# Kernel optimization log

Measured on AMD Instinct MI355X. Metric: run time of the kernel, lower is better.

## Reference

```python
import jax, jax.numpy as jnp
import numpy as np

N, E, IN_FEATS, D, H, DIST_DIM, NBOUND = 10000, 160000, 128, 64, 4, 32, 31

def setup_inputs() -> dict:
    key = jax.random.key(0)
    ks = jax.random.split(key, 16)
    gain = 5.0 / 3.0  # tanh gain
    def xavier(k, shape):
        # xavier_normal over the last two dims (fan_in, fan_out) as torch does per-slice
        fan_in, fan_out = shape[-2], shape[-1]
        std = gain * np.sqrt(2.0 / (fan_in + fan_out))
        return jax.random.normal(k, shape, dtype=jnp.float32) * std
    inp = {
        'feat': jax.random.normal(ks[0], (N, IN_FEATS), dtype=jnp.float32),
        'locations': jax.random.normal(ks[1], (N, 3), dtype=jnp.float32),
        'src': jax.random.randint(ks[2], (E,), 0, N),
        'dst': jax.random.randint(ks[3], (E,), 0, N),
        'inter_ids': jax.random.randint(ks[4], (E, H), 0, N),
        'W_fc': xavier(ks[5], (IN_FEATS, H * D)),
        'embed_table': jax.random.normal(ks[6], (NBOUND + 1, DIST_DIM), dtype=jnp.float32),
        'G': xavier(ks[7], (H, DIST_DIM, D)),
        'attn_fc1': xavier(ks[8], (H, 2 * D, D)),
        'attn_fc2': xavier(ks[9], (H, 2 * D, D)),
        'attn_fc3': xavier(ks[10], (H, 2 * D, D)),
        'attn_fc': xavier(ks[11], (H, 3 * D, D)),
        'attn_out': xavier(ks[12], (H, D, 1)),
        'boundaries': jnp.linspace(0.1, 3.1, NBOUND).astype(jnp.float32),
    }
    return inp


def reference(feat, locations, W_fc, embed_table, G, attn_fc1, attn_fc2, attn_fc3,
              attn_fc, attn_out, boundaries, src, dst, inter_ids):
    n = feat.shape[0]
    h = (feat @ W_fc).reshape(n, H, D)                      # [N,H,D]
    pos = locations                                          # [N,3]
    src_pos = pos[src]                                       # [E,3]
    dst_pos = pos[dst]                                       # [E,3]
    inter_pos = pos[inter_ids]                               # [E,H,3]
    h_src = h[src]                                           # [E,H,D]
    h_dst = h[dst]                                           # [E,H,D]
    head_idx = jnp.arange(H)[None, :]
    inter_h = h[inter_ids, head_idx, :]                      # [E,H,D] per-head gather

    e_count = src.shape[0]
    dist1 = jnp.broadcast_to(jnp.linalg.norm(dst_pos - src_pos, axis=-1)[:, None], (e_count, H))
    dist2 = jnp.linalg.norm(dst_pos[:, None, :] - inter_pos, axis=-1)   # [E,H]
    dist_ = jnp.linalg.norm(src_pos[:, None, :] - inter_pos, axis=-1)   # [E,H]

    def dist_embed(dist):
        idx = jnp.searchsorted(boundaries, dist, side='left')  # torch.bucketize(right=False)
        e = embed_table[idx]                                   # [E,H,DIST_DIM]
        return jnp.einsum('ehk,hkd->ehd', e, G)                # [E,H,D]

    de1 = dist_embed(dist1)
    de2 = dist_embed(dist2)
    de_ = dist_embed(dist_)

    d1 = jnp.einsum('ehk,hkd->ehd', jnp.concatenate([h_src, de1], axis=-1), attn_fc1)
    d2 = jnp.einsum('ehk,hkd->ehd', jnp.concatenate([inter_h, de2], axis=-1), attn_fc2)
    d3 = jnp.einsum('ehk,hkd->ehd', jnp.concatenate([h_dst, de_], axis=-1), attn_fc3)

    h_c = jnp.tanh(jnp.einsum('ehk,hkd->ehd', jnp.concatenate([d1, d2, d3], axis=-1), attn_fc))
    e_score = jnp.einsum('ehd,hdo->eho', h_c, attn_out)[..., 0]        # [E,H]

    # edge softmax grouped by destination node
    m = jax.ops.segment_max(e_score, dst, num_segments=n)              # [N,H]
    ex = jnp.exp(e_score - m[dst])
    den = jax.ops.segment_sum(ex, dst, num_segments=n)                 # [N,H]
    a = ex / den[dst]                                                  # [E,H]

    ft = jax.ops.segment_sum(a[:, :, None] * h_src, dst, num_segments=n)  # [N,H,D]
    rst = jnp.mean(ft, axis=1)                                          # merge='mean' -> [N,D]
    return rst
```

## Files before the change

kernel.cpp:

```cpp
#include <hip/hip_runtime.h>
#include <hip/hip_fp16.h>
#include <math.h>

#define N_NODES 10000
#define E_EDGES 160000
#define DMODEL 64
#define H 4
#define NBOUND 31
#define SLOTS 64
#define QREC 1024

typedef _Float16 half8 __attribute__((ext_vector_type(8)));
typedef float floatx4 __attribute__((ext_vector_type(4)));

__device__ __forceinline__ void mm4(const float* __restrict__ S, int aoff,
                                    int astride, int boff, int i0, int j,
                                    int Kdim, float o[4]) {
  float a0 = 0.f, a1 = 0.f, a2 = 0.f, a3 = 0.f;
  for (int t4 = 0; t4 < (Kdim >> 2); ++t4) {
    float4 f0 = *(const float4*)&S[aoff + (i0 + 0) * astride + t4 * 4];
    float4 f1 = *(const float4*)&S[aoff + (i0 + 1) * astride + t4 * 4];
    float4 f2 = *(const float4*)&S[aoff + (i0 + 2) * astride + t4 * 4];
    float4 f3 = *(const float4*)&S[aoff + (i0 + 3) * astride + t4 * 4];
    float b0 = S[boff + (t4 * 4 + 0) * 64 + j];
    float b1 = S[boff + (t4 * 4 + 1) * 64 + j];
    float b2 = S[boff + (t4 * 4 + 2) * 64 + j];
    float b3 = S[boff + (t4 * 4 + 3) * 64 + j];
    a0 += f0.x * b0 + f0.y * b1 + f0.z * b2 + f0.w * b3;
    a1 += f1.x * b0 + f1.y * b1 + f1.z * b2 + f1.w * b3;
    a2 += f2.x * b0 + f2.y * b1 + f2.z * b2 + f2.w * b3;
    a3 += f3.x * b0 + f3.y * b1 + f3.z * b2 + f3.w * b3;
  }
  o[0] = a0; o[1] = a1; o[2] = a2; o[3] = a3;
}

__device__ __forceinline__ int didx(const float* __restrict__ bnd2, float d) {
  int g = (int)(d * 10.0f);
  g = (g < 0) ? 0 : ((g > 31) ? 31 : g);
  g += (bnd2[g + 1] < d) ? 1 : 0;
  g -= (bnd2[g] >= d) ? 1 : 0;
  return g;
}

__global__ __launch_bounds__(512) void prep_kernel(
    const float* __restrict__ fc1, const float* __restrict__ fc2,
    const float* __restrict__ fc3, const float* __restrict__ fcc,
    const float* __restrict__ Wfc, const float* __restrict__ G,
    const float* __restrict__ emb, __half* __restrict__ bigWT,
    __half* __restrict__ U16, int* __restrict__ cnt) {
  __shared__ __align__(16) float S[12288];
  int bi = blockIdx.x;
  int tid = threadIdx.x;
  if (bi >= 24) {
    int n = (bi - 24) * 512 + tid;
    if (n < N_NODES) cnt[n] = 0;
    return;
  }
  int chain = (bi >= 12);
  int kh = chain ? (bi - 12) : bi;
  int k = kh >> 2, h = kh & 3;
  const float* fck = (k == 0) ? fc1 : (k == 1) ? fc2 : fc3;
  fck += h * 128 * 64;
  const float* F = fcc + h * 192 * 64 + k * 64 * 64;
  int j = tid & 63, ig = tid >> 6;
  float o[4];
  if (!chain) {
    #pragma unroll
    for (int u = 0; u < 2; ++u) {
      ((float4*)S)[u * 512 + tid] = ((const float4*)F)[u * 512 + tid];
      ((float4*)(S + 4096))[u * 512 + tid] = ((const float4*)fck)[u * 512 + tid];
    }
    __syncthreads();
    #pragma unroll
    for (int rg = 0; rg < 2; ++rg) {
      int i0 = ig * 8 + rg * 4;
      mm4(S, 4096, 64, 0, i0, j, 64, o);
      S[8192 + (i0 + 0) * 64 + j] = o[0];
      S[8192 + (i0 + 1) * 64 + j] = o[1];
      S[8192 + (i0 + 2) * 64 + j] = o[2];
      S[8192 + (i0 + 3) * 64 + j] = o[3];
    }
    __syncthreads();
    #pragma unroll
    for (int u = 0; u < 2; ++u) {
      int fi = u * 512 + tid;
      int i = fi >> 4, c4 = fi & 15;
      ((float4*)(S + 4096))[fi] = ((const float4*)(Wfc + i * 256 + h * 64))[c4];
    }
    __syncthreads();
    if (k == 0) {
      #pragma unroll
      for (int u = 0; u < 8; ++u) {
        int idx = u * 512 + tid;
        int i = idx >> 6, jj = idx & 63;
        bigWT[(h * 64 + jj) * 128 + i] = __float2half(S[4096 + idx]);
      }
    }
    #pragma unroll
    for (int rg = 0; rg < 2; ++rg) {
      int i0 = ig * 8 + rg * 4;
      mm4(S, 4096, 64, 8192, i0, j, 64, o);
      int rb = ((k + 1) * 256 + h * 64 + j) * 128;
      bigWT[rb + i0 + 0] = __float2half(o[0]);
      bigWT[rb + i0 + 1] = __float2half(o[1]);
      bigWT[rb + i0 + 2] = __float2half(o[2]);
      bigWT[rb + i0 + 3] = __float2half(o[3]);
    }
    __syncthreads();
    #pragma unroll
    for (int u = 0; u < 2; ++u) {
      int fi = u * 512 + tid;
      int i = fi >> 4, c4 = fi & 15;
      ((float4*)(S + 4096))[fi] =
          ((const float4*)(Wfc + (64 + i) * 256 + h * 64))[c4];
    }
    __syncthreads();
    if (k == 0) {
      #pragma unroll
      for (int u = 0; u < 8; ++u) {
        int idx = u * 512 + tid;
        int i = idx >> 6, jj = idx & 63;
        bigWT[(h * 64 + jj) * 128 + 64 + i] = __float2half(S[4096 + idx]);
      }
    }
    #pragma unroll
    for (int rg = 0; rg < 2; ++rg) {
      int i0 = ig * 8 + rg * 4;
      mm4(S, 4096, 64, 8192, i0, j, 64, o);
      int rb = ((k + 1) * 256 + h * 64 + j) * 128;
      bigWT[rb + 64 + i0 + 0] = __float2half(o[0]);
      bigWT[rb + 64 + i0 + 1] = __float2half(o[1]);
      bigWT[rb + 64 + i0 + 2] = __float2half(o[2]);
      bigWT[rb + 64 + i0 + 3] = __float2half(o[3]);
    }
    return;
  }
  #pragma unroll
  for (int u = 0; u < 2; ++u) {
    ((float4*)S)[u * 512 + tid] = ((const float4*)F)[u * 512 + tid];
    ((float4*)(S + 4096))[u * 512 + tid] =
        ((const float4*)(fck + 4096))[u * 512 + tid];
  }
  __syncthreads();
  #pragma unroll
  for (int rg = 0; rg < 2; ++rg) {
    int i0 = ig * 8 + rg * 4;
    mm4(S, 4096, 64, 0, i0, j, 64, o);
    S[8192 + (i0 + 0) * 64 + j] = o[0];
    S[8192 + (i0 + 1) * 64 + j] = o[1];
    S[8192 + (i0 + 2) * 64 + j] = o[2];
    S[8192 + (i0 + 3) * 64 + j] = o[3];
  }
  __syncthreads();
  ((float4*)S)[tid] = ((const float4*)(G + h * 2048))[tid];
  if (tid < 256) ((float4*)(S + 2048))[tid] = ((const float4*)emb)[tid];
  __syncthreads();
  {
    int i0 = ig * 4;
    mm4(S, 0, 64, 8192, i0, j, 64, o);
    S[3072 + (i0 + 0) * 64 + j] = o[0];
    S[3072 + (i0 + 1) * 64 + j] = o[1];
    S[3072 + (i0 + 2) * 64 + j] = o[2];
    S[3072 + (i0 + 3) * 64 + j] = o[3];
  }
  __syncthreads();
  {
    int i0 = ig * 4;
    mm4(S, 2048, 32, 3072, i0, j, 32, o);
    int base = k * 8192 + h * 2048;
    U16[base + (i0 + 0) * 64 + j] = __float2half(o[0]);
    U16[base + (i0 + 1) * 64 + j] = __float2half(o[1]);
    U16[base + (i0 + 2) * 64 + j] = __float2half(o[2]);
    U16[base + (i0 + 3) * 64 + j] = __float2half(o[3]);
  }
}

#define EROW 264

__global__ __launch_bounds__(256) void gemm_edge_kernel(
    const float* __restrict__ feat, const __half* __restrict__ bigWT,
    __half* __restrict__ qall, const float* __restrict__ pos,
    const int* __restrict__ src, const int* __restrict__ dst,
    const int* __restrict__ inter, const float* __restrict__ boundaries,
    int* __restrict__ cnt, uint4* __restrict__ ebuf) {
  __shared__ __align__(16) __half Esm[4][16][EROW];
  __shared__ float Sb[48];
  int bi = blockIdx.x;
  int tid = threadIdx.x;
  if (bi >= 628) {
    if (tid < NBOUND) Sb[tid + 1] = boundaries[tid];
    if (tid == NBOUND) { Sb[0] = -INFINITY; Sb[32] = INFINITY; }
    __syncthreads();
    int e = (bi - 628) * 256 + tid;
    int s = src[e], t = dst[e];
    int4 iv = *(const int4*)&inter[e * 4];
    int itarr[4] = {iv.x, iv.y, iv.z, iv.w};
    float sx = pos[s * 3], sy = pos[s * 3 + 1], sz = pos[s * 3 + 2];
    float tx = pos[t * 3], ty = pos[t * 3 + 1], tz = pos[t * 3 + 2];
    float dx = tx - sx, dy = ty - sy, dz = tz - sz;
    float dist1 = sqrtf(dx * dx + dy * dy + dz * dz);
    unsigned i1 = (unsigned)didx(Sb, dist1);
    unsigned w3 = 0, q20 = 0, q_0 = 0;
    #pragma unroll
    for (int hh = 0; hh < 4; ++hh) {
      int it = itarr[hh];
      float ix = pos[it * 3], iy = pos[it * 3 + 1], iz = pos[it * 3 + 2];
      float ax = tx - ix, ay = ty - iy, az = tz - iz;
      float dist2 = sqrtf(ax * ax + ay * ay + az * az);
      float bx = sx - ix, by = sy - iy, bz = sz - iz;
      float dist_ = sqrtf(bx * bx + by * by + bz * bz);
      unsigned idx2 = (unsigned)didx(Sb, dist2);
      unsigned idx_ = (unsigned)didx(Sb, dist_);
      if (hh == 0) { q20 = idx2; q_0 = idx_; }
      else w3 |= (idx2 | (idx_ << 5)) << ((hh - 1) * 10);
    }
    uint4 rec;
    rec.x = (unsigned)s | ((unsigned)itarr[0] << 16);
    rec.y = (unsigned)itarr[1] | ((unsigned)itarr[2] << 16);
    rec.z = (unsigned)itarr[3] | (i1 << 16) | (q20 << 21) | (q_0 << 26);
    rec.w = w3;
    int p = atomicAdd(&cnt[t], 1);
    if (p < SLOTS) ebuf[t * SLOTS + p] = rec;
    return;
  }
  int bx = bi % 157, by = bi / 157;
  int wv = tid >> 6, l = tid & 63;
  int m0 = bx * 64 + wv * 16;
  int n0 = by * 256;
  int lm = l & 15, lk = (l >> 4) * 8;
  int arow = m0 + lm;
  if (arow >= N_NODES) arow = N_NODES - 1;
  const float* fp = feat + arow * 128 + lk;
  const _Float16* bp = (const _Float16*)bigWT + lk;
  half8 a[4];
  #pragma unroll
  for (int kt = 0; kt < 4; ++kt) {
    float4 u0 = *(const float4*)(fp + kt * 32);
    float4 u1 = *(const float4*)(fp + kt * 32 + 4);
    half8 t;
    t[0] = (_Float16)u0.x; t[1] = (_Float16)u0.y;
    t[2] = (_Float16)u0.z; t[3] = (_Float16)u0.w;
    t[4] = (_Float16)u1.x; t[5] = (_Float16)u1.y;
    t[6] = (_Float16)u1.z; t[7] = (_Float16)u1.w;
    a[kt] = t;
  }
  #pragma unroll
  for (int nt = 0; nt < 16; ++nt) {
    floatx4 acc = (floatx4){0.f, 0.f, 0.f, 0.f};
    #pragma unroll
    for (int kt = 0; kt < 4; ++kt) {
      half8 b = *(const half8*)(bp + (n0 + nt * 16 + lm) * 128 + kt * 32);
      acc = __builtin_amdgcn_mfma_f32_16x16x32_f16(a[kt], b, acc, 0, 0, 0);
    }
    int dd = nt * 16 + lm;
    int o = (by == 0) ? ((dd & 63) * 4 + (dd >> 6)) : dd;
    #pragma unroll
    for (int r4 = 0; r4 < 4; ++r4)
      Esm[wv][(l >> 4) * 4 + r4][o] = __float2half(acc[r4]);
  }
  __syncthreads();
  int row = l >> 2;
  int j0 = (l & 3) * 64;
  int m = m0 + row;
  if (m < N_NODES) {
    #pragma unroll
    for (int u = 0; u < 8; ++u) {
      uint4 v = *(const uint4*)&Esm[wv][row][j0 + u * 8];
      *(uint4*)&qall[m * QREC + by * 256 + j0 + u * 8] = v;
    }
  }
}

__device__ __forceinline__ float dpp_row_sum16(float v) {
  int x;
  x = __builtin_amdgcn_update_dpp(0, __float_as_int(v), 0x128, 0xf, 0xf, true);
  v += __int_as_float(x);
  x = __builtin_amdgcn_update_dpp(0, __float_as_int(v), 0x124, 0xf, 0xf, true);
  v += __int_as_float(x);
  x = __builtin_amdgcn_update_dpp(0, __float_as_int(v), 0x122, 0xf, 0xf, true);
  v += __int_as_float(x);
  x = __builtin_amdgcn_update_dpp(0, __float_as_int(v), 0x121, 0xf, 0xf, true);
  v += __int_as_float(x);
  return v;
}

union H4u { uint2 u; __half2 h[2]; };

__device__ __forceinline__ float tanh_dot(H4u A, H4u B, H4u C, H4u X, H4u Y,
                                          H4u Z, float4 a4) {
  __half2 z0 = __hadd2(__hadd2(A.h[0], B.h[0]), __hadd2(C.h[0], X.h[0]));
  z0 = __hadd2(z0, __hadd2(Y.h[0], Z.h[0]));
  __half2 z1 = __hadd2(__hadd2(A.h[1], B.h[1]), __hadd2(C.h[1], X.h[1]));
  z1 = __hadd2(z1, __hadd2(Y.h[1], Z.h[1]));
  float2 f0 = __half22float2(z0);
  float2 f1 = __half22float2(z1);
  const float K = 2.885390082f;
  float p0 = __builtin_amdgcn_exp2f(f0.x * K);
  float p1 = __builtin_amdgcn_exp2f(f0.y * K);
  float p2 = __builtin_amdgcn_exp2f(f1.x * K);
  float p3 = __builtin_amdgcn_exp2f(f1.y * K);
  float r0 = __builtin_amdgcn_rcpf(p0 + 1.0f);
  float r1 = __builtin_amdgcn_rcpf(p1 + 1.0f);
  float r2 = __builtin_amdgcn_rcpf(p2 + 1.0f);
  float r3 = __builtin_amdgcn_rcpf(p3 + 1.0f);
  float dot = a4.x * r0;
  dot = fmaf(a4.y, r1, dot);
  dot = fmaf(a4.z, r2, dot);
  dot = fmaf(a4.w, r3, dot);
  float asum = (a4.x + a4.y) + (a4.z + a4.w);
  return fmaf(-2.0f, dot, asum);
}

__device__ __forceinline__ float4 h4_to_f4(uint2 u) {
  union { uint2 ui; __half2 h[2]; } cc;
  cc.ui = u;
  float2 a = __half22float2(cc.h[0]);
  float2 b = __half22float2(cc.h[1]);
  return make_float4(a.x, a.y, b.x, b.y);
}

__device__ __forceinline__ void dec_rec(uint4 r, int h, int* s, int* it,
                                        unsigned* i1, unsigned* q2,
                                        unsigned* q_) {
  *s = (int)(r.x & 0xffff);
  *it = (h == 0) ? (int)(r.x >> 16)
      : (h == 1) ? (int)(r.y & 0xffff)
      : (h == 2) ? (int)(r.y >> 16) : (int)(r.z & 0xffff);
  *i1 = (r.z >> 16) & 31;
  if (h == 0) {
    *q2 = (r.z >> 21) & 31;
    *q_ = (r.z >> 26) & 31;
  } else {
    unsigned f = r.w >> ((h - 1) * 10);
    *q2 = f & 31;
    *q_ = (f >> 5) & 31;
  }
}

__device__ __forceinline__ void gather_edge(
    const __half* __restrict__ qall, const __half* __restrict__ U16, int h,
    int c, int lane, int s, int it, unsigned i1, unsigned q2, unsigned q_,
    H4u* A, H4u* B, H4u* X, H4u* Y, H4u* Z, uint2* hr) {
  A->u = *(const uint2*)(qall + s * QREC + 256 + h * 64 + c * 4);
  B->u = *(const uint2*)(qall + it * QREC + 512 + h * 64 + c * 4);
  X->u = *(const uint2*)(U16 + (h * 32 + (int)i1) * 64 + c * 4);
  Y->u = *(const uint2*)(U16 + 8192 + (h * 32 + (int)q2) * 64 + c * 4);
  Z->u = *(const uint2*)(U16 + 16384 + (h * 32 + (int)q_) * 64 + c * 4);
  *hr = *(const uint2*)(qall + s * QREC + lane * 4);
}

__global__ __launch_bounds__(256) void score_agg_kernel(
    const int* __restrict__ cnt, const uint4* __restrict__ ebuf,
    const __half* __restrict__ qall, const __half* __restrict__ U16,
    const float* __restrict__ aout, float* __restrict__ out) {
  __shared__ uint4 recs[SLOTS];
  __shared__ float4 sm_num[4][64];
  __shared__ float4 sm_den[4];
  int tid = threadIdx.x;
  int w = tid >> 6, lane = tid & 63;
  int h = lane >> 4, c = lane & 15;
  int n = blockIdx.x;
  int deg = cnt[n];
  if (deg > SLOTS) deg = SLOTS;
  if (tid < deg) recs[tid] = ebuf[n * SLOTS + tid];
  H4u C;
  C.u = *(const uint2*)(qall + n * QREC + 768 + h * 64 + c * 4);
  const float4 a4 = *((const float4*)(aout + h * 64) + c);
  __syncthreads();
  float4 num = make_float4(0.f, 0.f, 0.f, 0.f);
  float4 den = make_float4(0.f, 0.f, 0.f, 0.f);
  for (int i = w; i < deg; i += 8) {
    int iB = i + 4;
    int vB = (iB < deg);
    uint4 rA = recs[i];
    uint4 rB = recs[vB ? iB : i];
    int sA, itA, sB, itB;
    unsigned i1A, q2A, q_A, i1B, q2B, q_B;
    dec_rec(rA, h, &sA, &itA, &i1A, &q2A, &q_A);
    dec_rec(rB, h, &sB, &itB, &i1B, &q2B, &q_B);
    H4u A0, B0, X0, Y0, Z0, A1, B1, X1, Y1, Z1;
    uint2 hr0, hr1;
    gather_edge(qall, U16, h, c, lane, sA, itA, i1A, q2A, q_A, &A0, &B0, &X0,
                &Y0, &Z0, &hr0);
    gather_edge(qall, U16, h, c, lane, sB, itB, i1B, q2B, q_B, &A1, &B1, &X1,
                &Y1, &Z1, &hr1);
    float v0 = tanh_dot(A0, B0, C, X0, Y0, Z0, a4);
    float v1 = tanh_dot(A1, B1, C, X1, Y1, Z1, a4);
    v0 = dpp_row_sum16(v0);
    v1 = dpp_row_sum16(v1);
    float ex0 = __expf(v0);
    float ex1 = vB ? __expf(v1) : 0.f;
    float4 hv0 = h4_to_f4(hr0);
    float4 hv1 = h4_to_f4(hr1);
    float e00 = __shfl(ex0, 0), e01 = __shfl(ex0, 16);
    float e02 = __shfl(ex0, 32), e03 = __shfl(ex0, 48);
    float e10 = __shfl(ex1, 0), e11 = __shfl(ex1, 16);
    float e12 = __shfl(ex1, 32), e13 = __shfl(ex1, 48);
    num.x += e00 * hv0.x + e10 * hv1.x;
    num.y += e01 * hv0.y + e11 * hv1.y;
    num.z += e02 * hv0.z + e12 * hv1.z;
    num.w += e03 * hv0.w + e13 * hv1.w;
    den.x += e00 + e10;
    den.y += e01 + e11;
    den.z += e02 + e12;
    den.w += e03 + e13;
  }
  sm_num[w][lane] = num;
  if (lane == 0) sm_den[w] = den;
  __syncthreads();
  if (tid < 64) {
    float4 n0 = sm_num[0][tid], n1 = sm_num[1][tid];
    float4 n2 = sm_num[2][tid], n3 = sm_num[3][tid];
    float4 d0 = sm_den[0], d1 = sm_den[1], d2 = sm_den[2], d3 = sm_den[3];
    float4 ns = make_float4(n0.x + n1.x + n2.x + n3.x, n0.y + n1.y + n2.y + n3.y,
                            n0.z + n1.z + n2.z + n3.z, n0.w + n1.w + n2.w + n3.w);
    float4 ds = make_float4(d0.x + d1.x + d2.x + d3.x, d0.y + d1.y + d2.y + d3.y,
                            d0.z + d1.z + d2.z + d3.z, d0.w + d1.w + d2.w + d3.w);
    float r = 0.f;
    if (deg > 0)
      r = 0.25f * (ns.x / ds.x + ns.y / ds.y + ns.z / ds.z + ns.w / ds.w);
    out[n * 64 + tid] = r;
  }
}

extern "C" void kernel_launch(void* const* d_in, const int* in_sizes, int n_in,
                              void* d_out, int out_size, void* d_ws,
                              size_t ws_size, hipStream_t stream) {
  const float* feat = (const float*)d_in[0];
  const float* loc = (const float*)d_in[1];
  const int* src = (const int*)d_in[2];
  const int* dst = (const int*)d_in[3];
  const int* inter = (const int*)d_in[4];
  const float* Wfc = (const float*)d_in[5];
  const float* emb = (const float*)d_in[6];
  const float* G = (const float*)d_in[7];
  const float* fc1 = (const float*)d_in[8];
  const float* fc2 = (const float*)d_in[9];
  const float* fc3 = (const float*)d_in[10];
  const float* fcc = (const float*)d_in[11];
  const float* aout = (const float*)d_in[12];
  const float* bnd = (const float*)d_in[13];
  float* out = (float*)d_out;

  __half* qall = (__half*)d_ws;
  __half* bigWT = qall + N_NODES * QREC;
  __half* U16 = bigWT + 1024 * 128;
  uint4* ebuf = (uint4*)(U16 + 3 * H * 2048);
  int* cnt = (int*)(ebuf + N_NODES * SLOTS);

  prep_kernel<<<44, 512, 0, stream>>>(fc1, fc2, fc3, fcc, Wfc, G, emb, bigWT,
                                      U16, cnt);
  gemm_edge_kernel<<<1253, 256, 0, stream>>>(feat, bigWT, qall, loc, src, dst,
                                             inter, bnd, cnt, ebuf);
  score_agg_kernel<<<N_NODES, 256, 0, stream>>>(cnt, ebuf, qall, U16, aout,
                                                out);
}
```

Measured before the change: 174.4 us.

## Interleave source features with projections, pad positions, per-lane head aggregation

```diff
diff --git a/kernel.cpp b/kernel.cpp
--- a/kernel.cpp
+++ b/kernel.cpp
@@ -46,14 +46,18 @@
     const float* __restrict__ fc1, const float* __restrict__ fc2,
     const float* __restrict__ fc3, const float* __restrict__ fcc,
     const float* __restrict__ Wfc, const float* __restrict__ G,
-    const float* __restrict__ emb, __half* __restrict__ bigWT,
-    __half* __restrict__ U16, int* __restrict__ cnt) {
+    const float* __restrict__ emb, const float* __restrict__ pos,
+    __half* __restrict__ bigWT, __half* __restrict__ U16,
+    int* __restrict__ cnt, float4* __restrict__ pos4) {
   __shared__ __align__(16) float S[12288];
   int bi = blockIdx.x;
   int tid = threadIdx.x;
   if (bi >= 24) {
     int n = (bi - 24) * 512 + tid;
-    if (n < N_NODES) cnt[n] = 0;
+    if (n < N_NODES) {
+      cnt[n] = 0;
+      pos4[n] = make_float4(pos[n * 3], pos[n * 3 + 1], pos[n * 3 + 2], 0.f);
+    }
     return;
   }
   int chain = (bi >= 12);
@@ -179,7 +183,7 @@
 
 __global__ __launch_bounds__(256) void gemm_edge_kernel(
     const float* __restrict__ feat, const __half* __restrict__ bigWT,
-    __half* __restrict__ qall, const float* __restrict__ pos,
+    __half* __restrict__ qall, const float4* __restrict__ pos4,
     const int* __restrict__ src, const int* __restrict__ dst,
     const int* __restrict__ inter, const float* __restrict__ boundaries,
     int* __restrict__ cnt, uint4* __restrict__ ebuf) {
@@ -195,19 +199,18 @@
     int s = src[e], t = dst[e];
     int4 iv = *(const int4*)&inter[e * 4];
     int itarr[4] = {iv.x, iv.y, iv.z, iv.w};
-    float sx = pos[s * 3], sy = pos[s * 3 + 1], sz = pos[s * 3 + 2];
-    float tx = pos[t * 3], ty = pos[t * 3 + 1], tz = pos[t * 3 + 2];
-    float dx = tx - sx, dy = ty - sy, dz = tz - sz;
+    float4 sp = pos4[s];
+    float4 tp = pos4[t];
+    float dx = tp.x - sp.x, dy = tp.y - sp.y, dz = tp.z - sp.z;
     float dist1 = sqrtf(dx * dx + dy * dy + dz * dz);
     unsigned i1 = (unsigned)didx(Sb, dist1);
     unsigned w3 = 0, q20 = 0, q_0 = 0;
     #pragma unroll
     for (int hh = 0; hh < 4; ++hh) {
-      int it = itarr[hh];
-      float ix = pos[it * 3], iy = pos[it * 3 + 1], iz = pos[it * 3 + 2];
-      float ax = tx - ix, ay = ty - iy, az = tz - iz;
+      float4 ip = pos4[itarr[hh]];
+      float ax = tp.x - ip.x, ay = tp.y - ip.y, az = tp.z - ip.z;
       float dist2 = sqrtf(ax * ax + ay * ay + az * az);
-      float bx = sx - ix, by = sy - iy, bz = sz - iz;
+      float bx = sp.x - ip.x, by = sp.y - ip.y, bz = sp.z - ip.z;
       float dist_ = sqrtf(bx * bx + by * by + bz * bz);
       unsigned idx2 = (unsigned)didx(Sb, dist2);
       unsigned idx_ = (unsigned)didx(Sb, dist_);
@@ -253,38 +256,48 @@
       acc = __builtin_amdgcn_mfma_f32_16x16x32_f16(a[kt], b, acc, 0, 0, 0);
     }
     int dd = nt * 16 + lm;
-    int o = (by == 0) ? ((dd & 63) * 4 + (dd >> 6)) : dd;
     #pragma unroll
     for (int r4 = 0; r4 < 4; ++r4)
-      Esm[wv][(l >> 4) * 4 + r4][o] = __float2half(acc[r4]);
+      Esm[wv][(l >> 4) * 4 + r4][dd] = __float2half(acc[r4]);
   }
   __syncthreads();
   int row = l >> 2;
-  int j0 = (l & 3) * 64;
   int m = m0 + row;
   if (m < N_NODES) {
-    #pragma unroll
-    for (int u = 0; u < 8; ++u) {
-      uint4 v = *(const uint4*)&Esm[wv][row][j0 + u * 8];
-      *(uint4*)&qall[m * QREC + by * 256 + j0 + u * 8] = v;
-    }
-  }
-}
-
-__device__ __forceinline__ float dpp_row_sum16(float v) {
+    if (by >= 2) {
+      int j0 = (l & 3) * 64;
+      #pragma unroll
+      for (int u = 0; u < 8; ++u) {
+        uint4 v = *(const uint4*)&Esm[wv][row][j0 + u * 8];
+        *(uint4*)&qall[m * QREC + by * 256 + j0 + u * 8] = v;
+      }
+    } else {
+      int g0 = (l & 3) * 16;
+      #pragma unroll
+      for (int u = 0; u < 16; ++u) {
+        int g = g0 + u;
+        uint2 v = *(const uint2*)&Esm[wv][row][g * 4];
+        *(uint2*)&qall[m * QREC + g * 8 + by * 4] = v;
+      }
+    }
+  }
+}
+
+__device__ __forceinline__ float dpp_bfly_sum16(float v) {
   int x;
-  x = __builtin_amdgcn_update_dpp(0, __float_as_int(v), 0x128, 0xf, 0xf, true);
+  x = __builtin_amdgcn_update_dpp(0, __float_as_int(v), 0xB1, 0xf, 0xf, true);
   v += __int_as_float(x);
-  x = __builtin_amdgcn_update_dpp(0, __float_as_int(v), 0x124, 0xf, 0xf, true);
+  x = __builtin_amdgcn_update_dpp(0, __float_as_int(v), 0x4E, 0xf, 0xf, true);
   v += __int_as_float(x);
-  x = __builtin_amdgcn_update_dpp(0, __float_as_int(v), 0x122, 0xf, 0xf, true);
+  x = __builtin_amdgcn_update_dpp(0, __float_as_int(v), 0x141, 0xf, 0xf, true);
   v += __int_as_float(x);
-  x = __builtin_amdgcn_update_dpp(0, __float_as_int(v), 0x121, 0xf, 0xf, true);
+  x = __builtin_amdgcn_update_dpp(0, __float_as_int(v), 0x140, 0xf, 0xf, true);
   v += __int_as_float(x);
   return v;
 }
 
 union H4u { uint2 u; __half2 h[2]; };
+union H8u { uint4 u4; __half2 h2[4]; };
 
 __device__ __forceinline__ float tanh_dot(H4u A, H4u B, H4u C, H4u X, H4u Y,
                                           H4u Z, float4 a4) {
@@ -311,14 +324,6 @@
   return fmaf(-2.0f, dot, asum);
 }
 
-__device__ __forceinline__ float4 h4_to_f4(uint2 u) {
-  union { uint2 ui; __half2 h[2]; } cc;
-  cc.ui = u;
-  float2 a = __half22float2(cc.h[0]);
-  float2 b = __half22float2(cc.h[1]);
-  return make_float4(a.x, a.y, b.x, b.y);
-}
-
 __device__ __forceinline__ void dec_rec(uint4 r, int h, int* s, int* it,
                                         unsigned* i1, unsigned* q2,
                                         unsigned* q_) {
@@ -337,25 +342,13 @@
   }
 }
 
-__device__ __forceinline__ void gather_edge(
-    const __half* __restrict__ qall, const __half* __restrict__ U16, int h,
-    int c, int lane, int s, int it, unsigned i1, unsigned q2, unsigned q_,
-    H4u* A, H4u* B, H4u* X, H4u* Y, H4u* Z, uint2* hr) {
-  A->u = *(const uint2*)(qall + s * QREC + 256 + h * 64 + c * 4);
-  B->u = *(const uint2*)(qall + it * QREC + 512 + h * 64 + c * 4);
-  X->u = *(const uint2*)(U16 + (h * 32 + (int)i1) * 64 + c * 4);
-  Y->u = *(const uint2*)(U16 + 8192 + (h * 32 + (int)q2) * 64 + c * 4);
-  Z->u = *(const uint2*)(U16 + 16384 + (h * 32 + (int)q_) * 64 + c * 4);
-  *hr = *(const uint2*)(qall + s * QREC + lane * 4);
-}
-
 __global__ __launch_bounds__(256) void score_agg_kernel(
     const int* __restrict__ cnt, const uint4* __restrict__ ebuf,
     const __half* __restrict__ qall, const __half* __restrict__ U16,
     const float* __restrict__ aout, float* __restrict__ out) {
   __shared__ uint4 recs[SLOTS];
   __shared__ float4 sm_num[4][64];
-  __shared__ float4 sm_den[4];
+  __shared__ float sm_den[4][4];
   int tid = threadIdx.x;
   int w = tid >> 6, lane = tid & 63;
   int h = lane >> 4, c = lane & 15;
@@ -368,7 +361,7 @@
   const float4 a4 = *((const float4*)(aout + h * 64) + c);
   __syncthreads();
   float4 num = make_float4(0.f, 0.f, 0.f, 0.f);
-  float4 den = make_float4(0.f, 0.f, 0.f, 0.f);
+  float den = 0.f;
   for (int i = w; i < deg; i += 8) {
     int iB = i + 4;
     int vB = (iB < deg);
@@ -378,48 +371,61 @@
     unsigned i1A, q2A, q_A, i1B, q2B, q_B;
     dec_rec(rA, h, &sA, &itA, &i1A, &q2A, &q_A);
     dec_rec(rB, h, &sB, &itB, &i1B, &q2B, &q_B);
-    H4u A0, B0, X0, Y0, Z0, A1, B1, X1, Y1, Z1;
-    uint2 hr0, hr1;
-    gather_edge(qall, U16, h, c, lane, sA, itA, i1A, q2A, q_A, &A0, &B0, &X0,
-                &Y0, &Z0, &hr0);
-    gather_edge(qall, U16, h, c, lane, sB, itB, i1B, q2B, q_B, &A1, &B1, &X1,
-                &Y1, &Z1, &hr1);
+    int g8 = (h * 16 + c) * 8;
+    H8u AH0, AH1;
+    H4u B0, X0, Y0, Z0, B1, X1, Y1, Z1;
+    AH0.u4 = *(const uint4*)(qall + sA * QREC + g8);
+    B0.u = *(const uint2*)(qall + itA * QREC + 512 + h * 64 + c * 4);
+    X0.u = *(const uint2*)(U16 + (h * 32 + (int)i1A) * 64 + c * 4);
+    Y0.u = *(const uint2*)(U16 + 8192 + (h * 32 + (int)q2A) * 64 + c * 4);
+    Z0.u = *(const uint2*)(U16 + 16384 + (h * 32 + (int)q_A) * 64 + c * 4);
+    AH1.u4 = *(const uint4*)(qall + sB * QREC + g8);
+    B1.u = *(const uint2*)(qall + itB * QREC + 512 + h * 64 + c * 4);
+    X1.u = *(const uint2*)(U16 + (h * 32 + (int)i1B) * 64 + c * 4);
+    Y1.u = *(const uint2*)(U16 + 8192 + (h * 32 + (int)q2B) * 64 + c * 4);
+    Z1.u = *(const uint2*)(U16 + 16384 + (h * 32 + (int)q_B) * 64 + c * 4);
+    H4u A0, A1;
+    A0.h[0] = AH0.h2[2]; A0.h[1] = AH0.h2[3];
+    A1.h[0] = AH1.h2[2]; A1.h[1] = AH1.h2[3];
     float v0 = tanh_dot(A0, B0, C, X0, Y0, Z0, a4);
     float v1 = tanh_dot(A1, B1, C, X1, Y1, Z1, a4);
-    v0 = dpp_row_sum16(v0);
-    v1 = dpp_row_sum16(v1);
+    v0 = dpp_bfly_sum16(v0);
+    v1 = dpp_bfly_sum16(v1);
     float ex0 = __expf(v0);
     float ex1 = vB ? __expf(v1) : 0.f;
-    float4 hv0 = h4_to_f4(hr0);
-    float4 hv1 = h4_to_f4(hr1);
-    float e00 = __shfl(ex0, 0), e01 = __shfl(ex0, 16);
-    float e02 = __shfl(ex0, 32), e03 = __shfl(ex0, 48);
-    float e10 = __shfl(ex1, 0), e11 = __shfl(ex1, 16);
-    float e12 = __shfl(ex1, 32), e13 = __shfl(ex1, 48);
-    num.x += e00 * hv0.x + e10 * hv1.x;
-    num.y += e01 * hv0.y + e11 * hv1.y;
-    num.z += e02 * hv0.z + e12 * hv1.z;
-    num.w += e03 * hv0.w + e13 * hv1.w;
-    den.x += e00 + e10;
-    den.y += e01 + e11;
-    den.z += e02 + e12;
-    den.w += e03 + e13;
+    float2 h00 = __half22float2(AH0.h2[0]);
+    float2 h01 = __half22float2(AH0.h2[1]);
+    float2 h10 = __half22float2(AH1.h2[0]);
+    float2 h11 = __half22float2(AH1.h2[1]);
+    num.x += ex0 * h00.x + ex1 * h10.x;
+    num.y += ex0 * h00.y + ex1 * h10.y;
+    num.z += ex0 * h01.x + ex1 * h11.x;
+    num.w += ex0 * h01.y + ex1 * h11.y;
+    den += ex0 + ex1;
   }
   sm_num[w][lane] = num;
-  if (lane == 0) sm_den[w] = den;
+  if (c == 0) sm_den[w][h] = den;
   __syncthreads();
   if (tid < 64) {
-    float4 n0 = sm_num[0][tid], n1 = sm_num[1][tid];
-    float4 n2 = sm_num[2][tid], n3 = sm_num[3][tid];
-    float4 d0 = sm_den[0], d1 = sm_den[1], d2 = sm_den[2], d3 = sm_den[3];
-    float4 ns = make_float4(n0.x + n1.x + n2.x + n3.x, n0.y + n1.y + n2.y + n3.y,
-                            n0.z + n1.z + n2.z + n3.z, n0.w + n1.w + n2.w + n3.w);
-    float4 ds = make_float4(d0.x + d1.x + d2.x + d3.x, d0.y + d1.y + d2.y + d3.y,
-                            d0.z + d1.z + d2.z + d3.z, d0.w + d1.w + d2.w + d3.w);
-    float r = 0.f;
-    if (deg > 0)
-      r = 0.25f * (ns.x / ds.x + ns.y / ds.y + ns.z / ds.z + ns.w / ds.w);
-    out[n * 64 + tid] = r;
+    float4 n0 = sm_num[0][lane], n1 = sm_num[1][lane];
+    float4 n2 = sm_num[2][lane], n3 = sm_num[3][lane];
+    float dt = sm_den[0][h] + sm_den[1][h] + sm_den[2][h] + sm_den[3][h];
+    float4 t = make_float4(0.f, 0.f, 0.f, 0.f);
+    if (deg > 0) {
+      float inv = 1.0f / dt;
+      t.x = (n0.x + n1.x + n2.x + n3.x) * inv;
+      t.y = (n0.y + n1.y + n2.y + n3.y) * inv;
+      t.z = (n0.z + n1.z + n2.z + n3.z) * inv;
+      t.w = (n0.w + n1.w + n2.w + n3.w) * inv;
+    }
+    t.x += __shfl_xor(t.x, 16); t.y += __shfl_xor(t.y, 16);
+    t.z += __shfl_xor(t.z, 16); t.w += __shfl_xor(t.w, 16);
+    t.x += __shfl_xor(t.x, 32); t.y += __shfl_xor(t.y, 32);
+    t.z += __shfl_xor(t.z, 32); t.w += __shfl_xor(t.w, 32);
+    if (h == 0) {
+      t.x *= 0.25f; t.y *= 0.25f; t.z *= 0.25f; t.w *= 0.25f;
+      *(float4*)&out[n * 64 + c * 4] = t;
+    }
   }
 }
 
@@ -447,10 +453,11 @@
   __half* U16 = bigWT + 1024 * 128;
   uint4* ebuf = (uint4*)(U16 + 3 * H * 2048);
   int* cnt = (int*)(ebuf + N_NODES * SLOTS);
-
-  prep_kernel<<<44, 512, 0, stream>>>(fc1, fc2, fc3, fcc, Wfc, G, emb, bigWT,
-                                      U16, cnt);
-  gemm_edge_kernel<<<1253, 256, 0, stream>>>(feat, bigWT, qall, loc, src, dst,
+  float4* pos4 = (float4*)(cnt + N_NODES);
+
+  prep_kernel<<<44, 512, 0, stream>>>(fc1, fc2, fc3, fcc, Wfc, G, emb, loc,
+                                      bigWT, U16, cnt, pos4);
+  gemm_edge_kernel<<<1253, 256, 0, stream>>>(feat, bigWT, qall, pos4, src, dst,
                                              inter, bnd, cnt, ebuf);
   score_agg_kernel<<<N_NODES, 256, 0, stream>>>(cnt, ebuf, qall, U16, aout,
                                                 out);
```

Result: slower. 179.8 us (+3.1%).
